# Kernel optimization log

Measured on AMD Instinct MI355X. Metric: run time of the kernel, lower is better.

The kernel has to match this reference:

```python
import jax, jax.numpy as jnp
import numpy as np

NUM_FRAMES = 16
NUM_PATCHES = 196
EMBED = 768
BATCH = 8
RATIOS = np.array([0.25, 0.5, 0.25], dtype=np.float32)
DIAG_INDEX = 1


def _init_smoothing_matrix():
    """Banded (num_frames, num_frames) matrix: each row is RATIOS translated so that
    RATIOS[DIAG_INDEX] sits on the diagonal; rows normalized to sum to 1."""
    F = NUM_FRAMES
    k = len(RATIOS)
    M = np.zeros((F, F), dtype=np.float32)
    for i in range(F):  # loop over small fixed num_frames at setup time only
        start = i - DIAG_INDEX
        end = i + k - DIAG_INDEX
        ms, me = max(0, start), min(F, end)
        rs = max(0, -start)
        re = k - max(0, end - F)
        M[i, ms:me] = RATIOS[rs:re]
    M /= M.sum(axis=1, keepdims=True)
    return jnp.asarray(M)


def setup_inputs() -> dict:
    key = jax.random.key(0)
    x = jax.random.normal(key, (BATCH, NUM_FRAMES * NUM_PATCHES + 1, EMBED), dtype=jnp.float32)
    return {"x": x, "smoothing_matrix": _init_smoothing_matrix()}


def reference(x, smoothing_matrix):
    # x: (B, F*P + 1, E); x[:, 0] is the CLS token.
    B, _, E = x.shape
    cls_tokens = x[:, :1]
    patches = x[:, 1:].reshape(B, NUM_FRAMES, NUM_PATCHES, E)  # (B, F, P, E)
    # smoothed[t] = sum_f M[t, f] * patches[f]  -- banded temporal blend,
    # expressed as a small contraction over the frame axis (no O(F^2*P*E) broadcast).
    smoothed = jnp.einsum('tf,bfpe->btpe', smoothing_matrix, patches)
    return jnp.concatenate([cls_tokens, smoothed.reshape(B, -1, E)], axis=1)
```

## Files before the change

### kernel.cpp

```cpp
#include <hip/hip_runtime.h>


#define NFRAMES 16
#define NPATCH  196
#define EMBED   768
#define NBATCH  8
#define NTOKENS (NFRAMES * NPATCH + 1)
#define E4      (EMBED / 4)
#define FSTRIDE (NPATCH * E4)

#define COL_TOTAL (NBATCH * NPATCH * E4)
#define CLS_TOTAL (NBATCH * E4)

typedef float v4f __attribute__((ext_vector_type(4)));

__global__ void __launch_bounds__(256)
patch_blender_col_nt_kernel(const v4f* __restrict__ x,
                            const float* __restrict__ M,
                            v4f* __restrict__ out) {
    __shared__ float sWl[NFRAMES], sWc[NFRAMES], sWr[NFRAMES];
    if (threadIdx.x < NFRAMES) {
        int t = threadIdx.x;
        sWl[t] = (t > 0)           ? M[t * NFRAMES + t - 1] : 0.0f;
        sWc[t] =                     M[t * NFRAMES + t];
        sWr[t] = (t < NFRAMES - 1) ? M[t * NFRAMES + t + 1] : 0.0f;
    }
    __syncthreads();

    int idx = blockIdx.x * blockDim.x + threadIdx.x;

    if (idx < COL_TOTAL) {
        int e4   = idx % E4;
        int rest = idx / E4;
        int p    = rest % NPATCH;
        int b    = rest / NPATCH;

        const size_t base = (size_t)b * NTOKENS * E4 + (size_t)(1 + p) * E4 + e4;

        v4f v[NFRAMES];
#pragma unroll
        for (int f = 0; f < NFRAMES; ++f)
            v[f] = x[base + (size_t)f * FSTRIDE];

#pragma unroll
        for (int t = 0; t < NFRAMES; ++t) {
            v4f a = sWc[t] * v[t];
            if (t > 0)           a += sWl[t] * v[t - 1];
            if (t < NFRAMES - 1) a += sWr[t] * v[t + 1];
            __builtin_nontemporal_store(a, &out[base + (size_t)t * FSTRIDE]);
        }
    } else if (idx < COL_TOTAL + CLS_TOTAL) {
        int j  = idx - COL_TOTAL;
        int e4 = j % E4;
        int b  = j / E4;
        size_t o = (size_t)b * NTOKENS * E4 + e4;
        v4f c = x[o];
        __builtin_nontemporal_store(c, &out[o]);
    }
}

extern "C" void kernel_launch(void* const* d_in, const int* in_sizes, int n_in,
                              void* d_out, int out_size, void* d_ws, size_t ws_size,
                              hipStream_t stream) {
    const v4f* x = (const v4f*)d_in[0];
    const float* M = (const float*)d_in[1];
    v4f* out = (v4f*)d_out;

    const int total = COL_TOTAL + CLS_TOTAL;
    int threads = 256;
    int blocks = (total + threads - 1) / threads;
    patch_blender_col_nt_kernel<<<blocks, threads, 0, stream>>>(x, M, out);
}
```

Baseline: 28.41 us.

## Stage frame columns in LDS and split frames across four thread groups

Each block now handles 64 columns across all 16 frames. The block stages the loaded values in a shared-memory tile, and each thread loads and writes only 4 frames instead of 16. This lowers register pressure and raises the number of loads in flight per block, at the cost of a block-wide barrier and LDS traffic. Nontemporal stores are replaced by ordinary stores, and the CLS copy moves to separate trailing blocks.

```diff
diff --git a/kernel.cpp b/kernel.cpp
--- a/kernel.cpp
+++ b/kernel.cpp
@@ -9,53 +9,68 @@
 #define E4      (EMBED / 4)
 #define FSTRIDE (NPATCH * E4)
 
-#define COL_TOTAL (NBATCH * NPATCH * E4)
+#define NCOLS    (NBATCH * NPATCH * E4)
+#define CPB      64
+#define NPBLOCKS (NCOLS / CPB)
 #define CLS_TOTAL (NBATCH * E4)
+#define NCBLOCKS ((CLS_TOTAL + 255) / 256)
 
 typedef float v4f __attribute__((ext_vector_type(4)));
 
 __global__ void __launch_bounds__(256)
-patch_blender_col_nt_kernel(const v4f* __restrict__ x,
-                            const float* __restrict__ M,
-                            v4f* __restrict__ out) {
+patch_blender_lds_kernel(const v4f* __restrict__ x,
+                         const float* __restrict__ M,
+                         v4f* __restrict__ out) {
+    int blk = blockIdx.x;
+    int tid = threadIdx.x;
+
+    if (blk >= NPBLOCKS) {
+        int j = (blk - NPBLOCKS) * 256 + tid;
+        if (j < CLS_TOTAL) {
+            int e4 = j % E4;
+            int b  = j / E4;
+            size_t o = (size_t)b * NTOKENS * E4 + e4;
+            out[o] = x[o];
+        }
+        return;
+    }
+
     __shared__ float sWl[NFRAMES], sWc[NFRAMES], sWr[NFRAMES];
-    if (threadIdx.x < NFRAMES) {
-        int t = threadIdx.x;
+    __shared__ v4f tile[NFRAMES][CPB];
+
+    if (tid < NFRAMES) {
+        int t = tid;
         sWl[t] = (t > 0)           ? M[t * NFRAMES + t - 1] : 0.0f;
         sWc[t] =                     M[t * NFRAMES + t];
         sWr[t] = (t < NFRAMES - 1) ? M[t * NFRAMES + t + 1] : 0.0f;
     }
+
+    int col0 = blk * CPB;
+    int e4_0 = col0 % E4;
+    int p    = (col0 / E4) % NPATCH;
+    int b    = col0 / (E4 * NPATCH);
+
+    int c  = tid & 63;
+    int tb = tid >> 6;
+
+    const size_t base = (size_t)b * NTOKENS * E4 + (size_t)(1 + p) * E4 + e4_0 + c;
+
+#pragma unroll
+    for (int i = 0; i < 4; ++i) {
+        int t = tb + 4 * i;
+        tile[t][c] = x[base + (size_t)t * FSTRIDE];
+    }
     __syncthreads();
 
-    int idx = blockIdx.x * blockDim.x + threadIdx.x;
-
-    if (idx < COL_TOTAL) {
-        int e4   = idx % E4;
-        int rest = idx / E4;
-        int p    = rest % NPATCH;
-        int b    = rest / NPATCH;
-
-        const size_t base = (size_t)b * NTOKENS * E4 + (size_t)(1 + p) * E4 + e4;
-
-        v4f v[NFRAMES];
 #pragma unroll
-        for (int f = 0; f < NFRAMES; ++f)
-            v[f] = x[base + (size_t)f * FSTRIDE];
-
-#pragma unroll
-        for (int t = 0; t < NFRAMES; ++t) {
-            v4f a = sWc[t] * v[t];
-            if (t > 0)           a += sWl[t] * v[t - 1];
-            if (t < NFRAMES - 1) a += sWr[t] * v[t + 1];
-            __builtin_nontemporal_store(a, &out[base + (size_t)t * FSTRIDE]);
-        }
-    } else if (idx < COL_TOTAL + CLS_TOTAL) {
-        int j  = idx - COL_TOTAL;
-        int e4 = j % E4;
-        int b  = j / E4;
-        size_t o = (size_t)b * NTOKENS * E4 + e4;
-        v4f c = x[o];
-        __builtin_nontemporal_store(c, &out[o]);
+    for (int i = 0; i < 4; ++i) {
+        int t  = tb + 4 * i;
+        int tl = (t == 0)           ? 0           : t - 1;
+        int tr = (t == NFRAMES - 1) ? NFRAMES - 1 : t + 1;
+        v4f a = sWc[t] * tile[t][c];
+        a += sWl[t] * tile[tl][c];
+        a += sWr[t] * tile[tr][c];
+        out[base + (size_t)t * FSTRIDE] = a;
     }
 }
 
@@ -66,8 +81,6 @@
     const float* M = (const float*)d_in[1];
     v4f* out = (v4f*)d_out;
 
-    const int total = COL_TOTAL + CLS_TOTAL;
-    int threads = 256;
-    int blocks = (total + threads - 1) / threads;
-    patch_blender_col_nt_kernel<<<blocks, threads, 0, stream>>>(x, M, out);
+    int blocks = NPBLOCKS + NCBLOCKS;
+    patch_blender_lds_kernel<<<blocks, 256, 0, stream>>>(x, M, out);
 }
```

Result: no change. 28.01 us (-1.4%).
